# Kernel tuning notes

Measured on AMD Instinct MI355X. Metric: run time of the kernel, lower is better.

The kernel has to match this reference:

```python
import jax, jax.numpy as jnp
import numpy as np

HIDDEN = 512
HEADS = 8
HEAD_DIM = HIDDEN // HEADS


def setup_inputs() -> dict:
    key = jax.random.key(0)
    ks = jax.random.split(key, 7)
    B, C, H, W = 8, HIDDEN, 32, 32
    scale = 1.0 / np.sqrt(C)
    inputs = jax.random.normal(ks[0], (B, C, H, W), dtype=jnp.float32)
    # 1x1 conv == per-pixel linear; store weights as [C_in, C_out]
    wq = jax.random.normal(ks[1], (C, HIDDEN), dtype=jnp.float32) * scale
    wk = jax.random.normal(ks[2], (C, HIDDEN), dtype=jnp.float32) * scale
    wv = jax.random.normal(ks[3], (C, HIDDEN), dtype=jnp.float32) * scale
    bq = jax.random.normal(ks[4], (HIDDEN,), dtype=jnp.float32) * 0.01
    bk = jax.random.normal(ks[5], (HIDDEN,), dtype=jnp.float32) * 0.01
    bv = jax.random.normal(ks[6], (HIDDEN,), dtype=jnp.float32) * 0.01
    return {"inputs": inputs, "wq": wq, "bq": bq, "wk": wk, "bk": bk, "wv": wv, "bv": bv}


def _proj_heads(x, w, b):
    # x: [B,C,H,W] -> tokens [B,heads,N,head_dim], matching transpose_for_scores
    B, C, H, W = x.shape
    t = jnp.einsum('bchw,cd->bhwd', x, w) + b          # [B,H,W,HIDDEN]
    t = t.reshape(B, H * W, HEADS, HEAD_DIM)
    return t.transpose(0, 2, 1, 3)                      # [B,heads,N,hd]


def reference(inputs, wq, bq, wk, bk, wv, bv):
    B, C, H, W = inputs.shape
    q = _proj_heads(inputs, wq, bq)
    k = _proj_heads(inputs, wk, bk)
    v = _proj_heads(inputs, wv, bv)
    # NOTE: original module applies NO 1/sqrt(d) scaling
    scores = jnp.einsum('bhnd,bhmd->bhnm', q, k)        # [B,heads,N,N]
    probs = jax.nn.softmax(scores, axis=-1)
    ctx = jnp.einsum('bhnm,bhmd->bhnd', probs, v)       # [B,heads,N,hd]
    # [B,heads,N,hd] -> [B,N,heads*hd] -> [B,H,W,C] -> [B,C,H,W]
    out = ctx.transpose(0, 2, 1, 3).reshape(B, H, W, HEADS * HEAD_DIM)
    return out.transpose(0, 3, 1, 2)
```

## Files before the change

kernel.cpp:

```cpp
#include <hip/hip_runtime.h>
#include <hip/hip_bf16.h>
#include <cmath>

#define B_     8
#define C_     512
#define N_     1024
#define HEADS_ 8
#define HD_    64
#define INST_  64

typedef short     v8s __attribute__((ext_vector_type(8)));
typedef _Float16  v8h __attribute__((ext_vector_type(8)));
typedef float    v16f __attribute__((ext_vector_type(16)));
typedef unsigned short ushort_t;
typedef unsigned int   uint_t;

__device__ inline ushort_t f2h(float x) {
    _Float16 h = (_Float16)x;
    ushort_t r; __builtin_memcpy(&r, &h, 2); return r;
}
__device__ inline uint_t pkbf(float a, float b) {
    __hip_bfloat162 p = __float22bfloat162_rn(make_float2(a, b));
    uint_t r; __builtin_memcpy(&r, &p, 4); return r;
}

__global__ __launch_bounds__(256) void prep_kernel(
    const float* __restrict__ x,
    const float* __restrict__ wq, const float* __restrict__ wk,
    const float* __restrict__ wv,
    uint_t* __restrict__ wt, uint_t* __restrict__ xt)
{
    __shared__ uint_t LH[64 * 32];
    const int z = blockIdx.z;
    const float* src;
    int srcStride;
    size_t outRow0;
    uint_t* oh;
    if (z < 3) {
        if (blockIdx.x >= 8) return;
        src = (z == 0) ? wq : (z == 1) ? wk : wv;
        srcStride = 512;
        outRow0 = (size_t)z * 512 + blockIdx.x * 64;
        oh = wt;
    } else {
        int b = z - 3;
        src = x + (size_t)b * C_ * N_;
        srcStride = 1024;
        outRow0 = (size_t)b * 1024 + blockIdx.x * 64;
        oh = xt;
    }
    const int d0 = blockIdx.x * 64;
    const int c0 = blockIdx.y * 64;
    const int t  = threadIdx.x;

    #pragma unroll
    for (int rep = 0; rep < 2; ++rep) {
        int idx = rep * 256 + t;
        int cp  = idx >> 4;
        int dq  = idx & 15;
        float4 fa = *(const float4*)&src[(size_t)(c0 + 2 * cp) * srcStride + d0 + dq * 4];
        float4 fb = *(const float4*)&src[(size_t)(c0 + 2 * cp + 1) * srcStride + d0 + dq * 4];
        float aa[4] = {fa.x, fa.y, fa.z, fa.w};
        float bb[4] = {fb.x, fb.y, fb.z, fb.w};
        #pragma unroll
        for (int j = 0; j < 4; ++j) {
            int d_l = dq * 4 + j;
            LH[d_l * 32 + (cp ^ (d_l & 31))] =
                (uint_t)f2h(aa[j]) | ((uint_t)f2h(bb[j]) << 16);
        }
    }
    __syncthreads();

    const int d_l = t >> 2;
    const int wq4 = (t & 3) * 8;
    uint_t vh[8];
    #pragma unroll
    for (int i = 0; i < 8; ++i)
        vh[i] = LH[d_l * 32 + ((wq4 + i) ^ (d_l & 31))];
    size_t base = (outRow0 + d_l) * 256 + c0 / 2 + wq4;
    *(uint4*)&oh[base]     = *(uint4*)&vh[0];
    *(uint4*)&oh[base + 4] = *(uint4*)&vh[4];
}

__global__ __launch_bounds__(256) void proj_kernel(
    const _Float16* __restrict__ xt, const _Float16* __restrict__ wt,
    const float* __restrict__ bq, const float* __restrict__ bk,
    const float* __restrict__ bv,
    ushort_t* __restrict__ qf, ushort_t* __restrict__ kf,
    ushort_t* __restrict__ vt)
{
    __shared__ _Float16 POOL[8192];
    _Float16* As = POOL;
    _Float16* Bs = POOL + 2048;

    const int tok0  = blockIdx.x * 64;
    const int b     = tok0 >> 10;
    const int ntb   = tok0 & 1023;
    const int by    = blockIdx.y;
    const int which = by >> 2;
    const int nloc0 = (by & 3) * 128;

    const int t   = threadIdx.x;
    const int w   = t >> 6;
    const int l   = t & 63;
    const int l31 = l & 31;
    const int h5  = l >> 5;
    const int wm  = w & 1;
    const int wn  = w >> 1;

    const int g   = t & 3;
    const int r0  = t >> 2;
    const int swz = g ^ (r0 & 3);

    const _Float16* baseA = xt + (size_t)(tok0 + r0) * 512 + g * 8;
    const _Float16* baseB = wt + (size_t)(which * 512 + nloc0 + r0) * 512 + g * 8;

    v8h pfa, pfb0, pfb1;
    auto load_tile = [&](int k0) {
        pfa  = *(const v8h*)(baseA + k0);
        pfb0 = *(const v8h*)(baseB + k0);
        pfb1 = *(const v8h*)(baseB + 32768 + k0);
    };
    auto store_tile = [&]() {
        *(v8h*)&As[(r0 * 4 + swz) * 8] = pfa;
        *(v8h*)&Bs[(r0 * 4 + swz) * 8] = pfb0;
        int row = 64 + r0;
        *(v8h*)&Bs[(row * 4 + (g ^ (row & 3))) * 8] = pfb1;
    };

    v16f acc[2] = {{}, {}};

    load_tile(0);
    store_tile();
    __syncthreads();

    for (int step = 0; step < 16; ++step) {
        if (step < 15) load_tile((step + 1) * 32);

        #pragma unroll
        for (int kc = 0; kc < 2; ++kc) {
            int rm = wm * 32 + l31;
            v8h af = *(const v8h*)&As[(rm * 4 + ((kc * 2 + h5) ^ (rm & 3))) * 8];
            v8h bf[2];
            #pragma unroll
            for (int ns = 0; ns < 2; ++ns) {
                int rn = wn * 64 + ns * 32 + l31;
                bf[ns] = *(const v8h*)&Bs[(rn * 4 + ((kc * 2 + h5) ^ (rn & 3))) * 8];
            }
            #pragma unroll
            for (int ns = 0; ns < 2; ++ns)
                acc[ns] = __builtin_amdgcn_mfma_f32_32x32x16_f16(
                    af, bf[ns], acc[ns], 0, 0, 0);
        }

        __syncthreads();
        if (step < 15) {
            store_tile();
            __syncthreads();
        }
    }

    if (which < 2) {
        ushort_t* oh = (which == 0) ? qf : kf;
        const float* bias = (which == 0) ? bq : bk;
        #pragma unroll
        for (int ns = 0; ns < 2; ++ns) {
            int d_local = nloc0 + wn * 64 + ns * 32 + l31;
            float bvv  = bias[d_local];
            int head   = d_local >> 6;
            int hd     = d_local & 63;
            size_t pb  = (size_t)(b * HEADS_ + head) * 65536 + hd;
            #pragma unroll
            for (int r = 0; r < 16; ++r) {
                int n = ntb + wm * 32 + (r & 3) + 8 * (r >> 2) + 4 * h5;
                oh[pb + (size_t)n * 64] = f2h(acc[ns][r] + bvv);
            }
        }
    } else {
        float bvv[2];
        #pragma unroll
        for (int ns = 0; ns < 2; ++ns)
            bvv[ns] = bv[nloc0 + wn * 64 + ns * 32 + l31];
        __syncthreads();
        uint_t* TW = (uint_t*)POOL + w * 1024;
        #pragma unroll
        for (int ns = 0; ns < 2; ++ns)
            #pragma unroll
            for (int r = 0; r < 16; r += 2) {
                int tok_l = (r & 3) + 8 * (r >> 2) + 4 * h5;
                int hd_l  = ns * 32 + l31;
                TW[hd_l * 16 + ((tok_l >> 1) ^ (hd_l & 15))] =
                    pkbf(acc[ns][r] + bvv[ns], acc[ns][r + 1] + bvv[ns]);
            }
        __syncthreads();
        const int head = (nloc0 + wn * 64) >> 6;
        uint_t* vtu = (uint_t*)vt;
        size_t base = (size_t)(b * HEADS_ + head) * 32768 + (size_t)l * 512
                    + (ntb + wm * 32) / 2;
        #pragma unroll
        for (int c = 0; c < 4; ++c) {
            uint_t wd[4];
            #pragma unroll
            for (int kk = 0; kk < 4; ++kk) {
                int wsx = c * 4 + kk;
                int w3 = wsx & 7;
                int sw = (wsx & ~7) | (w3 & 1) | (((w3 >> 1) & 1) << 2)
                                   | (((w3 >> 2) & 1) << 1);
                wd[kk] = TW[l * 16 + (sw ^ (l & 15))];
            }
            *(uint4*)&vtu[base + c * 4] = *(uint4*)&wd[0];
        }
    }
}

__global__ __launch_bounds__(256) void attn_kernel(
    const ushort_t* __restrict__ qf, const ushort_t* __restrict__ kf,
    const ushort_t* __restrict__ vt, float* __restrict__ out)
{
    __shared__ _Float16 KH[4096];
    __shared__ ushort_t VT[4096];
    __shared__ float    RS[128];

    const int inst  = blockIdx.x;
    const int chunk = blockIdx.y;
    const int t     = threadIdx.x;
    const int w     = t >> 6;
    const int l     = t & 63;
    const int l31   = l & 31;
    const int h5    = l >> 5;

    const ushort_t* Qf = qf + (size_t)inst * 65536;
    const ushort_t* Kf = kf + (size_t)inst * 65536;
    const ushort_t* Vt = vt + (size_t)inst * 65536;

    const int qbase = chunk * 128 + w * 32;

    v8h aq[4];
    #pragma unroll
    for (int ks = 0; ks < 4; ++ks)
        aq[ks] = *(const v8h*)&Qf[(size_t)(qbase + l31) * 64 + ks * 16 + h5 * 8];

    const int g   = t & 7;
    const int r0  = t >> 3;
    const int swz = g ^ (r0 & 7);
    const ushort_t* baseK = Kf + (size_t)r0 * 64 + g * 8;
    const ushort_t* baseV = Vt + (size_t)r0 * 1024 + g * 8;

    v8h pk0, pk1; v8s pv0, pv1;
    auto load_tile = [&](int kt) {
        pk0 = *(const v8h*)(baseK + (size_t)kt * 4096);
        pk1 = *(const v8h*)(baseK + (size_t)kt * 4096 + 2048);
        pv0 = *(const v8s*)(baseV + (size_t)kt * 64);
        pv1 = *(const v8s*)(baseV + 32768 + (size_t)kt * 64);
    };
    auto store_tile = [&]() {
        int so0 = (r0 * 8 + swz) * 8;
        int so1 = ((32 + r0) * 8 + swz) * 8;
        *(v8h*)&KH[so0] = pk0;
        *(v8h*)&KH[so1] = pk1;
        *(v8s*)&VT[so0] = pv0;
        *(v8s*)&VT[so1] = pv1;
    };

    v16f O0 = {}, O1 = {};
    float rsumv = 0.f;

    load_tile(0);
    store_tile();
    __syncthreads();

    for (int kt = 0; kt < 16; ++kt) {
        if (kt < 15) load_tile(kt + 1);

        #pragma unroll
        for (int t2 = 0; t2 < 2; ++t2) {
            v16f s = {};
            int kvrow = t2 * 32 + l31;
            #pragma unroll
            for (int ks = 0; ks < 4; ++ks) {
                int so = (kvrow * 8 + ((ks * 2 + h5) ^ (kvrow & 7))) * 8;
                v8h khf = *(const v8h*)&KH[so];
                s = __builtin_amdgcn_mfma_f32_32x32x16_f16(khf, aq[ks], s, 0, 0, 0);
            }
            float e0[8], e1[8];
            #pragma unroll
            for (int j = 0; j < 8; ++j) {
                e0[j] = __expf(s[j] - 64.0f);
                e1[j] = __expf(s[8 + j] - 64.0f);
                rsumv += e0[j] + e1[j];
            }
            uint4 u0, u1;
            u0.x = pkbf(e0[0], e0[1]); u0.y = pkbf(e0[2], e0[3]);
            u0.z = pkbf(e0[4], e0[5]); u0.w = pkbf(e0[6], e0[7]);
            u1.x = pkbf(e1[0], e1[1]); u1.y = pkbf(e1[2], e1[3]);
            u1.z = pkbf(e1[4], e1[5]); u1.w = pkbf(e1[6], e1[7]);
            v8s p0 = __builtin_bit_cast(v8s, u0);
            v8s p1 = __builtin_bit_cast(v8s, u1);

            #pragma unroll
            for (int hh = 0; hh < 2; ++hh) {
                int rv = hh * 32 + l31;
                int g0 = (4 * t2 + h5)     ^ (rv & 7);
                int g1 = (4 * t2 + 2 + h5) ^ (rv & 7);
                v8s bv0 = *(const v8s*)&VT[(rv * 8 + g0) * 8];
                v8s bv1 = *(const v8s*)&VT[(rv * 8 + g1) * 8];
                if (hh == 0) {
                    O0 = __builtin_amdgcn_mfma_f32_32x32x16_bf16(p0, bv0, O0, 0, 0, 0);
                    O0 = __builtin_amdgcn_mfma_f32_32x32x16_bf16(p1, bv1, O0, 0, 0, 0);
                } else {
                    O1 = __builtin_amdgcn_mfma_f32_32x32x16_bf16(p0, bv0, O1, 0, 0, 0);
                    O1 = __builtin_amdgcn_mfma_f32_32x32x16_bf16(p1, bv1, O1, 0, 0, 0);
                }
            }
        }

        __syncthreads();
        if (kt < 15) {
            store_tile();
            __syncthreads();
        }
    }

    float tot = rsumv + __shfl_xor(rsumv, 32, 64);
    if (h5 == 0) RS[w * 32 + l31] = 1.0f / tot;
    __syncthreads();
    float invr[16];
    #pragma unroll
    for (int r = 0; r < 16; ++r)
        invr[r] = RS[w * 32 + (r & 3) + 8 * (r >> 2) + 4 * h5];

    const int b    = inst >> 3;
    const int head = inst & 7;
    float* ob = out + (size_t)b * C_ * N_;
    #pragma unroll
    for (int hh = 0; hh < 2; ++hh) {
        const v16f& O = hh ? O1 : O0;
        int c = head * 64 + hh * 32 + l31;
        #pragma unroll
        for (int qd = 0; qd < 4; ++qd) {
            int n = qbase + 8 * qd + 4 * h5;
            float4 o4;
            o4.x = O[qd * 4 + 0] * invr[qd * 4 + 0];
            o4.y = O[qd * 4 + 1] * invr[qd * 4 + 1];
            o4.z = O[qd * 4 + 2] * invr[qd * 4 + 2];
            o4.w = O[qd * 4 + 3] * invr[qd * 4 + 3];
            *(float4*)&ob[(size_t)c * N_ + n] = o4;
        }
    }
}

extern "C" void kernel_launch(void* const* d_in, const int* in_sizes, int n_in,
                              void* d_out, int out_size, void* d_ws, size_t ws_size,
                              hipStream_t stream) {
    const float* x  = (const float*)d_in[0];
    const float* wq = (const float*)d_in[1];
    const float* bq = (const float*)d_in[2];
    const float* wk = (const float*)d_in[3];
    const float* bk = (const float*)d_in[4];
    const float* wv = (const float*)d_in[5];
    const float* bv = (const float*)d_in[6];
    float* out = (float*)d_out;

    char* ws = (char*)d_ws;
    _Float16* wt = (_Float16*)(ws);
    _Float16* xt = (_Float16*)(ws + 1572864);
    ushort_t* qf = (ushort_t*)(ws + 9961472);
    ushort_t* kf = (ushort_t*)(ws + 18350080);
    ushort_t* vt = (ushort_t*)(ws + 26738688);

    prep_kernel<<<dim3(16, 8, 11), 256, 0, stream>>>(
        x, wq, wk, wv, (uint_t*)wt, (uint_t*)xt);
    proj_kernel<<<dim3(128, 12), 256, 0, stream>>>(xt, wt, bq, bk, bv,
                                                   qf, kf, vt);
    attn_kernel<<<dim3(64, 8), 256, 0, stream>>>(qf, kf, vt, out);
}
```

Before: 140.1 us.

## Fuse input transpose/convert into projection GEMM and add MFMA priority hints

```diff
diff --git a/kernel.cpp b/kernel.cpp
--- a/kernel.cpp
+++ b/kernel.cpp
@@ -25,30 +25,15 @@
 }
 
 __global__ __launch_bounds__(256) void prep_kernel(
-    const float* __restrict__ x,
     const float* __restrict__ wq, const float* __restrict__ wk,
     const float* __restrict__ wv,
-    uint_t* __restrict__ wt, uint_t* __restrict__ xt)
+    uint_t* __restrict__ wt)
 {
     __shared__ uint_t LH[64 * 32];
     const int z = blockIdx.z;
-    const float* src;
-    int srcStride;
-    size_t outRow0;
-    uint_t* oh;
-    if (z < 3) {
-        if (blockIdx.x >= 8) return;
-        src = (z == 0) ? wq : (z == 1) ? wk : wv;
-        srcStride = 512;
-        outRow0 = (size_t)z * 512 + blockIdx.x * 64;
-        oh = wt;
-    } else {
-        int b = z - 3;
-        src = x + (size_t)b * C_ * N_;
-        srcStride = 1024;
-        outRow0 = (size_t)b * 1024 + blockIdx.x * 64;
-        oh = xt;
-    }
+    const float* src = (z == 0) ? wq : (z == 1) ? wk : wv;
+    const size_t outRow0 = (size_t)z * 512 + blockIdx.x * 64;
+
     const int d0 = blockIdx.x * 64;
     const int c0 = blockIdx.y * 64;
     const int t  = threadIdx.x;
@@ -58,8 +43,8 @@
         int idx = rep * 256 + t;
         int cp  = idx >> 4;
         int dq  = idx & 15;
-        float4 fa = *(const float4*)&src[(size_t)(c0 + 2 * cp) * srcStride + d0 + dq * 4];
-        float4 fb = *(const float4*)&src[(size_t)(c0 + 2 * cp + 1) * srcStride + d0 + dq * 4];
+        float4 fa = *(const float4*)&src[(size_t)(c0 + 2 * cp) * 512 + d0 + dq * 4];
+        float4 fb = *(const float4*)&src[(size_t)(c0 + 2 * cp + 1) * 512 + d0 + dq * 4];
         float aa[4] = {fa.x, fa.y, fa.z, fa.w};
         float bb[4] = {fb.x, fb.y, fb.z, fb.w};
         #pragma unroll
@@ -78,12 +63,12 @@
     for (int i = 0; i < 8; ++i)
         vh[i] = LH[d_l * 32 + ((wq4 + i) ^ (d_l & 31))];
     size_t base = (outRow0 + d_l) * 256 + c0 / 2 + wq4;
-    *(uint4*)&oh[base]     = *(uint4*)&vh[0];
-    *(uint4*)&oh[base + 4] = *(uint4*)&vh[4];
+    *(uint4*)&((uint_t*)wt)[base]     = *(uint4*)&vh[0];
+    *(uint4*)&((uint_t*)wt)[base + 4] = *(uint4*)&vh[4];
 }
 
 __global__ __launch_bounds__(256) void proj_kernel(
-    const _Float16* __restrict__ xt, const _Float16* __restrict__ wt,
+    const float* __restrict__ x, const _Float16* __restrict__ wt,
     const float* __restrict__ bq, const float* __restrict__ bk,
     const float* __restrict__ bv,
     ushort_t* __restrict__ qf, ushort_t* __restrict__ kf,
@@ -92,6 +77,7 @@
     __shared__ _Float16 POOL[8192];
     _Float16* As = POOL;
     _Float16* Bs = POOL + 2048;
+    uint_t*   Asu = (uint_t*)POOL;
 
     const int tok0  = blockIdx.x * 64;
     const int b     = tok0 >> 10;
@@ -111,18 +97,29 @@
     const int g   = t & 3;
     const int r0  = t >> 2;
     const int swz = g ^ (r0 & 3);
-
-    const _Float16* baseA = xt + (size_t)(tok0 + r0) * 512 + g * 8;
     const _Float16* baseB = wt + (size_t)(which * 512 + nloc0 + r0) * 512 + g * 8;
 
-    v8h pfa, pfb0, pfb1;
-    auto load_tile = [&](int k0) {
-        pfa  = *(const v8h*)(baseA + k0);
-        pfb0 = *(const v8h*)(baseB + k0);
-        pfb1 = *(const v8h*)(baseB + 32768 + k0);
+    const int cp = t & 15;
+    const int tq = t >> 4;
+    const float* baseX = x + (size_t)b * 524288 + (size_t)(2 * cp) * 1024
+                       + ntb + 4 * tq;
+
+    float4 pfa0, pfa1; v8h pfb0, pfb1;
+    auto load_tile = [&](int s) {
+        pfa0 = *(const float4*)(baseX + (size_t)s * 32768);
+        pfa1 = *(const float4*)(baseX + (size_t)s * 32768 + 1024);
+        pfb0 = *(const v8h*)(baseB + s * 32);
+        pfb1 = *(const v8h*)(baseB + 32768 + s * 32);
     };
     auto store_tile = [&]() {
-        *(v8h*)&As[(r0 * 4 + swz) * 8] = pfa;
+        float a0[4] = {pfa0.x, pfa0.y, pfa0.z, pfa0.w};
+        float a1[4] = {pfa1.x, pfa1.y, pfa1.z, pfa1.w};
+        #pragma unroll
+        for (int i = 0; i < 4; ++i) {
+            int rm = 4 * tq + i;
+            Asu[rm * 16 + ((cp >> 2) ^ i) * 4 + (cp & 3)] =
+                (uint_t)f2h(a0[i]) | ((uint_t)f2h(a1[i]) << 16);
+        }
         *(v8h*)&Bs[(r0 * 4 + swz) * 8] = pfb0;
         int row = 64 + r0;
         *(v8h*)&Bs[(row * 4 + (g ^ (row & 3))) * 8] = pfb1;
@@ -135,7 +132,7 @@
     __syncthreads();
 
     for (int step = 0; step < 16; ++step) {
-        if (step < 15) load_tile((step + 1) * 32);
+        if (step < 15) load_tile(step + 1);
 
         #pragma unroll
         for (int kc = 0; kc < 2; ++kc) {
@@ -276,12 +273,14 @@
         for (int t2 = 0; t2 < 2; ++t2) {
             v16f s = {};
             int kvrow = t2 * 32 + l31;
+            __builtin_amdgcn_s_setprio(1);
             #pragma unroll
             for (int ks = 0; ks < 4; ++ks) {
                 int so = (kvrow * 8 + ((ks * 2 + h5) ^ (kvrow & 7))) * 8;
                 v8h khf = *(const v8h*)&KH[so];
                 s = __builtin_amdgcn_mfma_f32_32x32x16_f16(khf, aq[ks], s, 0, 0, 0);
             }
+            __builtin_amdgcn_s_setprio(0);
             float e0[8], e1[8];
             #pragma unroll
             for (int j = 0; j < 8; ++j) {
@@ -297,6 +296,7 @@
             v8s p0 = __builtin_bit_cast(v8s, u0);
             v8s p1 = __builtin_bit_cast(v8s, u1);
 
+            __builtin_amdgcn_s_setprio(1);
             #pragma unroll
             for (int hh = 0; hh < 2; ++hh) {
                 int rv = hh * 32 + l31;
@@ -312,6 +312,7 @@
                     O1 = __builtin_amdgcn_mfma_f32_32x32x16_bf16(p1, bv1, O1, 0, 0, 0);
                 }
             }
+            __builtin_amdgcn_s_setprio(0);
         }
 
         __syncthreads();
@@ -363,14 +364,12 @@
 
     char* ws = (char*)d_ws;
     _Float16* wt = (_Float16*)(ws);
-    _Float16* xt = (_Float16*)(ws + 1572864);
     ushort_t* qf = (ushort_t*)(ws + 9961472);
     ushort_t* kf = (ushort_t*)(ws + 18350080);
     ushort_t* vt = (ushort_t*)(ws + 26738688);
 
-    prep_kernel<<<dim3(16, 8, 11), 256, 0, stream>>>(
-        x, wq, wk, wv, (uint_t*)wt, (uint_t*)xt);
-    proj_kernel<<<dim3(128, 12), 256, 0, stream>>>(xt, wt, bq, bk, bv,
+    prep_kernel<<<dim3(8, 8, 3), 256, 0, stream>>>(wq, wk, wv, (uint_t*)wt);
+    proj_kernel<<<dim3(128, 12), 256, 0, stream>>>(x, wt, bq, bk, bv,
                                                    qf, kf, vt);
     attn_kernel<<<dim3(64, 8), 256, 0, stream>>>(qf, kf, vt, out);
 }
```

New measurement: 147.9 us. +5.5%, slower.
